# Kernel tuning notes

Measured on AMD Instinct MI355X. Metric: run time of the kernel, lower is better.

Reference implementation:

```python
import jax, jax.numpy as jnp
import numpy as np

BS, NE, F = 128, 512, 6
HEADS, DPH = 4, 4
N_EMBD = HEADS * DPH  # 16


def setup_inputs() -> dict:
    key = jax.random.key(0)
    k_inp, k_mask, kq, kk, kv, kp = jax.random.split(key, 6)
    inp = jax.random.normal(k_inp, (BS, NE, F), dtype=jnp.float32)
    # binary float mask; guarantee at least one unmasked entity per batch row
    mask = (jax.random.uniform(k_mask, (BS, NE)) < 0.8).astype(jnp.float32)
    mask = mask.at[:, 0].set(1.0)
    std = 1.0 / np.sqrt(N_EMBD)
    Wq = jax.random.normal(kq, (N_EMBD, F), dtype=jnp.float32) * std
    Wk = jax.random.normal(kk, (N_EMBD, F), dtype=jnp.float32) * std
    Wv = jax.random.normal(kv, (N_EMBD, F), dtype=jnp.float32) * std
    Wpost = jax.random.normal(kp, (F, N_EMBD), dtype=jnp.float32) * std
    return {"inp": inp, "mask": mask, "Wq": Wq, "Wk": Wk, "Wv": Wv, "Wpost": Wpost}


def reference(inp, mask, Wq, Wk, Wv, Wpost):
    bs, ne, f = inp.shape
    x_in = inp * mask[:, :, None]                       # mask input entities
    # projections (Linear with weight [out,in]): x @ W.T
    q = (x_in @ Wq.T).reshape(bs, ne, HEADS, DPH)
    k = (x_in @ Wk.T).reshape(bs, ne, HEADS, DPH)
    v = (x_in @ Wv.T).reshape(bs, ne, HEADS, DPH)
    scale = 1.0 / np.sqrt(N_EMBD / HEADS)               # 1/sqrt(4)
    logits = jnp.einsum('bqhd,bkhd->bhqk', q, k) * scale  # [bs,H,NE,NE]
    logits = logits + 1e9 * (mask[:, None, None, :] - 1.0)  # mask keys pre-softmax
    p = jax.nn.softmax(logits, axis=-1)
    p = p * mask[:, None, :, None]                      # zero masked query rows
    att = jnp.einsum('bhqk,bkhd->bqhd', p, v).reshape(bs, ne, N_EMBD)
    x = x_in + att @ Wpost.T                            # residual
    # mask-corrected mean/std normalization over dims [1,2]
    N = jnp.sum(mask, axis=1)[:, None, None]            # [bs,1,1] valid entity count
    mu = jnp.mean(x, axis=(1, 2), keepdims=True) * (ne / N)
    x2 = x + (1.0 - mask[:, :, None]) * mu              # fill masked slots with mu
    m2 = jnp.mean(x2, axis=(1, 2), keepdims=True)
    var = jnp.sum((x2 - m2) ** 2, axis=(1, 2), keepdims=True) / (ne * f - 1)  # unbiased
    std = jnp.sqrt(var) * jnp.sqrt((f * ne - 1.0) / (f * N - 1.0))
    xn = (x - mu) / (std + 1e-6)
    # masked mean pool over entities
    summed = jnp.sum(xn * mask[:, :, None], axis=1)     # [bs,F]
    denom = jnp.sum(mask, axis=1)[:, None]
    return summed / denom
```

## Files before the change

kernel.cpp:

```cpp
#include <hip/hip_runtime.h>
#include <math.h>

#define BS    128
#define NE    512
#define F     6
#define NH    4
#define DPH   4
#define NEMBD 16

#define CH    8
#define CPAD  65

#if __has_builtin(__builtin_amdgcn_exp2f)
#define EXP2(x) __builtin_amdgcn_exp2f(x)
#else
#define EXP2(x) exp2f(x)
#endif

typedef float v2f __attribute__((ext_vector_type(2)));

__global__ __launch_bounds__(512) void attn_kernel(
    const float* __restrict__ inp, const float* __restrict__ mask,
    const float* __restrict__ Wq, const float* __restrict__ Wk,
    const float* __restrict__ Wv, float* __restrict__ att_out)
{
    const int b    = blockIdx.x >> 2;
    const int h    = blockIdx.x & 3;
    const int t    = threadIdx.x;
    const int c    = t & 7;
    const int g    = t >> 3;
    const int w    = t >> 6;
    const int lane = t & 63;

    __shared__ float4 sk[CH * CPAD];
    __shared__ float4 sv[CH * CPAD];
    __shared__ float4 sq[576];
    __shared__ unsigned short rlist[512];
    __shared__ int wcnt[8];

    const float4 z4 = make_float4(0.f, 0.f, 0.f, 0.f);
    sk[c * CPAD + g] = z4;
    sv[c * CPAD + g] = z4;
    sq[9 * g + c]    = z4;

    const float me = mask[b * NE + t];
    const bool act = me > 0.f;

    const unsigned long long ball = __ballot(act);
    const int prefix = __builtin_amdgcn_mbcnt_hi((unsigned int)(ball >> 32),
                        __builtin_amdgcn_mbcnt_lo((unsigned int)ball, 0));
    if (lane == 0) wcnt[w] = (int)__popcll(ball);

    __syncthreads();

    int base = 0, Nk = 0;
    #pragma unroll
    for (int u = 0; u < 8; ++u) {
        const int cu = wcnt[u];
        Nk += cu;
        if (u < w) base += cu;
    }
    const int L = (Nk + 7) >> 3;
    const float lcorr = (float)(8 * L - Nk);

    if (act) {
        const int s = base + prefix;
        const float2* rp = (const float2*)(inp + ((size_t)(b * NE + t)) * F);
        const float2 r0 = rp[0], r1 = rp[1], r2 = rp[2];
        const float x0 = r0.x, x1 = r0.y, x2 = r1.x,
                    x3 = r1.y, x4 = r2.x, x5 = r2.y;
        const float* wk = Wk + h * DPH * F;
        const float* wv = Wv + h * DPH * F;
        const float* wq = Wq + h * DPH * F;
        const float QS = 0.5f * 1.44269504088896340736f;
        float kk[4], vv[4], qq[4];
        #pragma unroll
        for (int d = 0; d < DPH; ++d) {
            const float* wd = wk + d * F;
            kk[d] = x0*wd[0] + x1*wd[1] + x2*wd[2] + x3*wd[3] + x4*wd[4] + x5*wd[5];
            wd = wv + d * F;
            vv[d] = x0*wd[0] + x1*wd[1] + x2*wd[2] + x3*wd[3] + x4*wd[4] + x5*wd[5];
            wd = wq + d * F;
            qq[d] = QS * (x0*wd[0] + x1*wd[1] + x2*wd[2] + x3*wd[3] + x4*wd[4] + x5*wd[5]);
        }
        sk[(s & 7) * CPAD + (s >> 3)] = make_float4(kk[0], kk[1], kk[2], kk[3]);
        sv[(s & 7) * CPAD + (s >> 3)] = make_float4(vv[0], vv[1], vv[2], vv[3]);
        sq[9 * (s >> 3) + (s & 7)]    = make_float4(qq[0], qq[1], qq[2], qq[3]);
        rlist[s] = (unsigned short)t;
    }

    __syncthreads();

    if (64 * w >= Nk) return;

    float4 qa[8];
    #pragma unroll
    for (int r = 0; r < 8; ++r) qa[r] = sq[9 * g + r];
    v2f qv[4][DPH];
    #pragma unroll
    for (int p = 0; p < 4; ++p) {
        qv[p][0] = (v2f){qa[2*p].x, qa[2*p+1].x};
        qv[p][1] = (v2f){qa[2*p].y, qa[2*p+1].y};
        qv[p][2] = (v2f){qa[2*p].z, qa[2*p+1].z};
        qv[p][3] = (v2f){qa[2*p].w, qa[2*p+1].w};
    }

    const float4* kb = sk + c * CPAD;
    const float4* vb = sv + c * CPAD;
    v2f l2[4], a2[4][DPH];
    #pragma unroll
    for (int p = 0; p < 4; ++p) {
        l2[p] = (v2f)(0.f);
        #pragma unroll
        for (int d = 0; d < DPH; ++d) a2[p][d] = (v2f)(0.f);
    }

    #pragma unroll 4
    for (int j = 0; j < L; ++j) {
        const float4 kv = kb[j];
        const float4 uv = vb[j];
        const v2f kx = (v2f){kv.x, kv.x}, ky = (v2f){kv.y, kv.y},
                  kz = (v2f){kv.z, kv.z}, kw = (v2f){kv.w, kv.w};
        const v2f ux = (v2f){uv.x, uv.x}, uy = (v2f){uv.y, uv.y},
                  uz = (v2f){uv.z, uv.z}, uw = (v2f){uv.w, uv.w};
        #pragma unroll
        for (int p = 0; p < 4; ++p) {
            v2f s = qv[p][3] * kw;
            s = __builtin_elementwise_fma(qv[p][2], kz, s);
            s = __builtin_elementwise_fma(qv[p][1], ky, s);
            s = __builtin_elementwise_fma(qv[p][0], kx, s);
            v2f e;
            e.x = EXP2(s.x);
            e.y = EXP2(s.y);
            l2[p] += e;
            a2[p][0] = __builtin_elementwise_fma(e, ux, a2[p][0]);
            a2[p][1] = __builtin_elementwise_fma(e, uy, a2[p][1]);
            a2[p][2] = __builtin_elementwise_fma(e, uz, a2[p][2]);
            a2[p][3] = __builtin_elementwise_fma(e, uw, a2[p][3]);
        }
    }

    const int b0 = c & 1, b1 = (c >> 1) & 1, b2 = (c >> 2) & 1;

    float k1[5][4];
    #pragma unroll
    for (int p = 0; p < 4; ++p) {
        {
            const v2f v = l2[p];
            const float snd = b0 ? v.x : v.y;
            k1[0][p] = (b0 ? v.y : v.x) + __shfl_xor(snd, 1);
        }
        #pragma unroll
        for (int d = 0; d < DPH; ++d) {
            const v2f v = a2[p][d];
            const float snd = b0 ? v.x : v.y;
            k1[1 + d][p] = (b0 ? v.y : v.x) + __shfl_xor(snd, 1);
        }
    }

    float k2[5][2];
    #pragma unroll
    for (int v = 0; v < 5; ++v) {
        #pragma unroll
        for (int q = 0; q < 2; ++q) {
            const float keep = b1 ? k1[v][2*q + 1] : k1[v][2*q];
            const float snd  = b1 ? k1[v][2*q]     : k1[v][2*q + 1];
            k2[v][q] = keep + __shfl_xor(snd, 2);
        }
    }

    float fin[5];
    #pragma unroll
    for (int v = 0; v < 5; ++v) {
        const float keep = b2 ? k2[v][1] : k2[v][0];
        const float snd  = b2 ? k2[v][0] : k2[v][1];
        fin[v] = keep + __shfl_xor(snd, 4);
    }

    const int slot = 8 * g + c;
    if (slot < Nk) {
        const int row = rlist[slot];
        const float rs = 1.0f / (fin[0] - lcorr);
        float4* o = (float4*)(att_out + ((size_t)(b * NE + row)) * NEMBD + h * DPH);
        *o = make_float4(fin[1] * rs, fin[2] * rs, fin[3] * rs, fin[4] * rs);
    }
}

__global__ __launch_bounds__(NE) void epi_kernel(
    const float* __restrict__ inp, const float* __restrict__ mask,
    const float* __restrict__ Wpost, const float* __restrict__ att,
    float* __restrict__ out)
{
    const int b = blockIdx.x;
    const int i = threadIdx.x;
    const int wave = i >> 6;
    const int lane = i & 63;

    __shared__ float swp[F * NEMBD];
    __shared__ float red[64];

    if (i < F * NEMBD) swp[i] = Wpost[i];
    __syncthreads();

    const float mi = mask[b * NE + i];
    const float* row = inp + ((size_t)(b * NE + i)) * F;
    const float* ar  = att + ((size_t)(b * NE + i)) * NEMBD;

    float a[NEMBD];
    #pragma unroll
    for (int t = 0; t < NEMBD; t += 4) {
        const float4 v = *(const float4*)(ar + t);
        a[t] = v.x * mi; a[t+1] = v.y * mi; a[t+2] = v.z * mi; a[t+3] = v.w * mi;
    }

    float x[F];
    #pragma unroll
    for (int f = 0; f < F; ++f) {
        float acc = row[f] * mi;
        #pragma unroll
        for (int t = 0; t < NEMBD; ++t) acc = fmaf(a[t], swp[f * NEMBD + t], acc);
        x[f] = acc;
    }

    float rsum = x[0] + x[1] + x[2] + x[3] + x[4] + x[5];
    float rn = mi;
    #pragma unroll
    for (int off = 32; off >= 1; off >>= 1) {
        rsum += __shfl_down(rsum, off);
        rn   += __shfl_down(rn, off);
    }
    if (lane == 0) { red[wave * 2] = rsum; red[wave * 2 + 1] = rn; }
    __syncthreads();
    float S = 0.f, N = 0.f;
    #pragma unroll
    for (int w = 0; w < 8; ++w) { S += red[w * 2]; N += red[w * 2 + 1]; }

    const float mu     = S / (6.0f * N);
    const float sum_x2 = S + (NE - N) * 6.0f * mu;
    const float m2     = sum_x2 / (NE * 6.0f);
    const float add    = (1.0f - mi) * mu;

    float ss = 0.f;
    #pragma unroll
    for (int f = 0; f < F; ++f) { const float d = x[f] + add - m2; ss = fmaf(d, d, ss); }

    __syncthreads();
    #pragma unroll
    for (int off = 32; off >= 1; off >>= 1) ss += __shfl_down(ss, off);
    if (lane == 0) red[wave] = ss;
    __syncthreads();
    float vs = 0.f;
    #pragma unroll
    for (int w = 0; w < 8; ++w) vs += red[w];

    const float var  = vs / (NE * 6.0f - 1.0f);
    const float stdv = sqrtf(var) * sqrtf((6.0f * NE - 1.0f) / (6.0f * N - 1.0f));
    const float inv  = 1.0f / (stdv + 1e-6f);

    float y[F];
    #pragma unroll
    for (int f = 0; f < F; ++f) y[f] = mi * (x[f] - mu) * inv;

    __syncthreads();
    #pragma unroll
    for (int off = 32; off >= 1; off >>= 1) {
        #pragma unroll
        for (int f = 0; f < F; ++f) y[f] += __shfl_down(y[f], off);
    }
    if (lane == 0) {
        #pragma unroll
        for (int f = 0; f < F; ++f) red[wave * F + f] = y[f];
    }
    __syncthreads();
    if (i < F) {
        float tt = 0.f;
        #pragma unroll
        for (int w = 0; w < 8; ++w) tt += red[w * F + i];
        out[b * F + i] = tt / N;
    }
}

extern "C" void kernel_launch(void* const* d_in, const int* in_sizes, int n_in,
                              void* d_out, int out_size, void* d_ws, size_t ws_size,
                              hipStream_t stream) {
    const float* inp   = (const float*)d_in[0];
    const float* mask  = (const float*)d_in[1];
    const float* Wq    = (const float*)d_in[2];
    const float* Wk    = (const float*)d_in[3];
    const float* Wv    = (const float*)d_in[4];
    const float* Wpost = (const float*)d_in[5];
    float* out = (float*)d_out;
    float* att = (float*)d_ws;

    attn_kernel<<<BS * NH, 512, 0, stream>>>(inp, mask, Wq, Wk, Wv, att);
    epi_kernel <<<BS, NE, 0, stream>>>(inp, mask, Wpost, att, out);
}
```

Measured before the change: 94.86 us.

## Fuse attention and epilogue kernels via per-batch atomic last-block completion

Merges the attention kernel and the normalization/pooling epilogue into one launch. Each of the four head-blocks for a batch row increments a global atomic counter, and the last one to finish runs the epilogue on the attention output the others wrote to global memory. This removes one kernel launch and the gap between the two kernels. In exchange it adds threadfence/atomic overhead, serializes the epilogue onto a single block per batch row, and adds a min-blocks launch-bounds hint. Correctness depends on the counter being reset at the end of each call.

```diff
diff --git a/kernel.cpp b/kernel.cpp
--- a/kernel.cpp
+++ b/kernel.cpp
@@ -19,10 +19,13 @@
 
 typedef float v2f __attribute__((ext_vector_type(2)));
 
-__global__ __launch_bounds__(512) void attn_kernel(
+__device__ int g_ctr[BS];
+
+__global__ __launch_bounds__(512, 4) void fused_kernel(
     const float* __restrict__ inp, const float* __restrict__ mask,
     const float* __restrict__ Wq, const float* __restrict__ Wk,
-    const float* __restrict__ Wv, float* __restrict__ att_out)
+    const float* __restrict__ Wv, const float* __restrict__ Wpost,
+    float* __restrict__ att_out, float* __restrict__ out)
 {
     const int b    = blockIdx.x >> 2;
     const int h    = blockIdx.x & 3;
@@ -37,6 +40,9 @@
     __shared__ float4 sq[576];
     __shared__ unsigned short rlist[512];
     __shared__ int wcnt[8];
+    __shared__ float swp[F * NEMBD];
+    __shared__ float red[64];
+    __shared__ int s_old;
 
     const float4 z4 = make_float4(0.f, 0.f, 0.f, 0.f);
     sk[c * CPAD + g] = z4;
@@ -91,126 +97,121 @@
 
     __syncthreads();
 
-    if (64 * w >= Nk) return;
-
-    float4 qa[8];
-    #pragma unroll
-    for (int r = 0; r < 8; ++r) qa[r] = sq[9 * g + r];
-    v2f qv[4][DPH];
-    #pragma unroll
-    for (int p = 0; p < 4; ++p) {
-        qv[p][0] = (v2f){qa[2*p].x, qa[2*p+1].x};
-        qv[p][1] = (v2f){qa[2*p].y, qa[2*p+1].y};
-        qv[p][2] = (v2f){qa[2*p].z, qa[2*p+1].z};
-        qv[p][3] = (v2f){qa[2*p].w, qa[2*p+1].w};
-    }
-
-    const float4* kb = sk + c * CPAD;
-    const float4* vb = sv + c * CPAD;
-    v2f l2[4], a2[4][DPH];
-    #pragma unroll
-    for (int p = 0; p < 4; ++p) {
-        l2[p] = (v2f)(0.f);
-        #pragma unroll
-        for (int d = 0; d < DPH; ++d) a2[p][d] = (v2f)(0.f);
-    }
-
-    #pragma unroll 4
-    for (int j = 0; j < L; ++j) {
-        const float4 kv = kb[j];
-        const float4 uv = vb[j];
-        const v2f kx = (v2f){kv.x, kv.x}, ky = (v2f){kv.y, kv.y},
-                  kz = (v2f){kv.z, kv.z}, kw = (v2f){kv.w, kv.w};
-        const v2f ux = (v2f){uv.x, uv.x}, uy = (v2f){uv.y, uv.y},
-                  uz = (v2f){uv.z, uv.z}, uw = (v2f){uv.w, uv.w};
+    if (64 * w < Nk) {
+        float4 qa[8];
+        #pragma unroll
+        for (int r = 0; r < 8; ++r) qa[r] = sq[9 * g + r];
+        v2f qv[4][DPH];
         #pragma unroll
         for (int p = 0; p < 4; ++p) {
-            v2f s = qv[p][3] * kw;
-            s = __builtin_elementwise_fma(qv[p][2], kz, s);
-            s = __builtin_elementwise_fma(qv[p][1], ky, s);
-            s = __builtin_elementwise_fma(qv[p][0], kx, s);
-            v2f e;
-            e.x = EXP2(s.x);
-            e.y = EXP2(s.y);
-            l2[p] += e;
-            a2[p][0] = __builtin_elementwise_fma(e, ux, a2[p][0]);
-            a2[p][1] = __builtin_elementwise_fma(e, uy, a2[p][1]);
-            a2[p][2] = __builtin_elementwise_fma(e, uz, a2[p][2]);
-            a2[p][3] = __builtin_elementwise_fma(e, uw, a2[p][3]);
-        }
-    }
-
-    const int b0 = c & 1, b1 = (c >> 1) & 1, b2 = (c >> 2) & 1;
-
-    float k1[5][4];
-    #pragma unroll
-    for (int p = 0; p < 4; ++p) {
-        {
-            const v2f v = l2[p];
-            const float snd = b0 ? v.x : v.y;
-            k1[0][p] = (b0 ? v.y : v.x) + __shfl_xor(snd, 1);
-        }
-        #pragma unroll
-        for (int d = 0; d < DPH; ++d) {
-            const v2f v = a2[p][d];
-            const float snd = b0 ? v.x : v.y;
-            k1[1 + d][p] = (b0 ? v.y : v.x) + __shfl_xor(snd, 1);
-        }
-    }
-
-    float k2[5][2];
-    #pragma unroll
-    for (int v = 0; v < 5; ++v) {
-        #pragma unroll
-        for (int q = 0; q < 2; ++q) {
-            const float keep = b1 ? k1[v][2*q + 1] : k1[v][2*q];
-            const float snd  = b1 ? k1[v][2*q]     : k1[v][2*q + 1];
-            k2[v][q] = keep + __shfl_xor(snd, 2);
-        }
-    }
-
-    float fin[5];
-    #pragma unroll
-    for (int v = 0; v < 5; ++v) {
-        const float keep = b2 ? k2[v][1] : k2[v][0];
-        const float snd  = b2 ? k2[v][0] : k2[v][1];
-        fin[v] = keep + __shfl_xor(snd, 4);
-    }
-
-    const int slot = 8 * g + c;
-    if (slot < Nk) {
-        const int row = rlist[slot];
-        const float rs = 1.0f / (fin[0] - lcorr);
-        float4* o = (float4*)(att_out + ((size_t)(b * NE + row)) * NEMBD + h * DPH);
-        *o = make_float4(fin[1] * rs, fin[2] * rs, fin[3] * rs, fin[4] * rs);
-    }
-}
-
-__global__ __launch_bounds__(NE) void epi_kernel(
-    const float* __restrict__ inp, const float* __restrict__ mask,
-    const float* __restrict__ Wpost, const float* __restrict__ att,
-    float* __restrict__ out)
-{
-    const int b = blockIdx.x;
-    const int i = threadIdx.x;
-    const int wave = i >> 6;
-    const int lane = i & 63;
-
-    __shared__ float swp[F * NEMBD];
-    __shared__ float red[64];
-
-    if (i < F * NEMBD) swp[i] = Wpost[i];
-    __syncthreads();
-
-    const float mi = mask[b * NE + i];
-    const float* row = inp + ((size_t)(b * NE + i)) * F;
-    const float* ar  = att + ((size_t)(b * NE + i)) * NEMBD;
+            qv[p][0] = (v2f){qa[2*p].x, qa[2*p+1].x};
+            qv[p][1] = (v2f){qa[2*p].y, qa[2*p+1].y};
+            qv[p][2] = (v2f){qa[2*p].z, qa[2*p+1].z};
+            qv[p][3] = (v2f){qa[2*p].w, qa[2*p+1].w};
+        }
+
+        const float4* kb = sk + c * CPAD;
+        const float4* vb = sv + c * CPAD;
+        v2f l2[4], a2[4][DPH];
+        #pragma unroll
+        for (int p = 0; p < 4; ++p) {
+            l2[p] = (v2f)(0.f);
+            #pragma unroll
+            for (int d = 0; d < DPH; ++d) a2[p][d] = (v2f)(0.f);
+        }
+
+        #pragma unroll 4
+        for (int j = 0; j < L; ++j) {
+            const float4 kv = kb[j];
+            const float4 uv = vb[j];
+            const v2f kx = (v2f){kv.x, kv.x}, ky = (v2f){kv.y, kv.y},
+                      kz = (v2f){kv.z, kv.z}, kw = (v2f){kv.w, kv.w};
+            const v2f ux = (v2f){uv.x, uv.x}, uy = (v2f){uv.y, uv.y},
+                      uz = (v2f){uv.z, uv.z}, uw = (v2f){uv.w, uv.w};
+            #pragma unroll
+            for (int p = 0; p < 4; ++p) {
+                v2f s = qv[p][3] * kw;
+                s = __builtin_elementwise_fma(qv[p][2], kz, s);
+                s = __builtin_elementwise_fma(qv[p][1], ky, s);
+                s = __builtin_elementwise_fma(qv[p][0], kx, s);
+                v2f e;
+                e.x = EXP2(s.x);
+                e.y = EXP2(s.y);
+                l2[p] += e;
+                a2[p][0] = __builtin_elementwise_fma(e, ux, a2[p][0]);
+                a2[p][1] = __builtin_elementwise_fma(e, uy, a2[p][1]);
+                a2[p][2] = __builtin_elementwise_fma(e, uz, a2[p][2]);
+                a2[p][3] = __builtin_elementwise_fma(e, uw, a2[p][3]);
+            }
+        }
+
+        const int b0 = c & 1, b1 = (c >> 1) & 1, b2 = (c >> 2) & 1;
+
+        float k1[5][4];
+        #pragma unroll
+        for (int p = 0; p < 4; ++p) {
+            {
+                const v2f v = l2[p];
+                const float snd = b0 ? v.x : v.y;
+                k1[0][p] = (b0 ? v.y : v.x) + __shfl_xor(snd, 1);
+            }
+            #pragma unroll
+            for (int d = 0; d < DPH; ++d) {
+                const v2f v = a2[p][d];
+                const float snd = b0 ? v.x : v.y;
+                k1[1 + d][p] = (b0 ? v.y : v.x) + __shfl_xor(snd, 1);
+            }
+        }
+
+        float k2[5][2];
+        #pragma unroll
+        for (int v = 0; v < 5; ++v) {
+            #pragma unroll
+            for (int q = 0; q < 2; ++q) {
+                const float keep = b1 ? k1[v][2*q + 1] : k1[v][2*q];
+                const float snd  = b1 ? k1[v][2*q]     : k1[v][2*q + 1];
+                k2[v][q] = keep + __shfl_xor(snd, 2);
+            }
+        }
+
+        float fin[5];
+        #pragma unroll
+        for (int v = 0; v < 5; ++v) {
+            const float keep = b2 ? k2[v][1] : k2[v][0];
+            const float snd  = b2 ? k2[v][0] : k2[v][1];
+            fin[v] = keep + __shfl_xor(snd, 4);
+        }
+
+        const int slot = 8 * g + c;
+        if (slot < Nk) {
+            const int row = rlist[slot];
+            const float rs = 1.0f / (fin[0] - lcorr);
+            float4* o = (float4*)(att_out + ((size_t)(b * NE + row)) * NEMBD + h * DPH);
+            *o = make_float4(fin[1] * rs, fin[2] * rs, fin[3] * rs, fin[4] * rs);
+        }
+    }
+
+    __syncthreads();
+    if (t == 0) {
+        __threadfence();
+        s_old = atomicAdd(&g_ctr[b], 1);
+    }
+    __syncthreads();
+    if (s_old != NH - 1) return;
+    __threadfence();
+
+    if (t < F * NEMBD) swp[t] = Wpost[t];
+    __syncthreads();
+
+    const float mi = me;
+    const float* row = inp + ((size_t)(b * NE + t)) * F;
+    const float* ar  = att_out + ((size_t)(b * NE + t)) * NEMBD;
 
     float a[NEMBD];
     #pragma unroll
-    for (int t = 0; t < NEMBD; t += 4) {
-        const float4 v = *(const float4*)(ar + t);
-        a[t] = v.x * mi; a[t+1] = v.y * mi; a[t+2] = v.z * mi; a[t+3] = v.w * mi;
+    for (int u = 0; u < NEMBD; u += 4) {
+        const float4 v = *(const float4*)(ar + u);
+        a[u] = v.x * mi; a[u+1] = v.y * mi; a[u+2] = v.z * mi; a[u+3] = v.w * mi;
     }
 
     float x[F];
@@ -218,7 +219,7 @@
     for (int f = 0; f < F; ++f) {
         float acc = row[f] * mi;
         #pragma unroll
-        for (int t = 0; t < NEMBD; ++t) acc = fmaf(a[t], swp[f * NEMBD + t], acc);
+        for (int u = 0; u < NEMBD; ++u) acc = fmaf(a[u], swp[f * NEMBD + u], acc);
         x[f] = acc;
     }
 
@@ -229,11 +230,11 @@
         rsum += __shfl_down(rsum, off);
         rn   += __shfl_down(rn, off);
     }
-    if (lane == 0) { red[wave * 2] = rsum; red[wave * 2 + 1] = rn; }
+    if (lane == 0) { red[w * 2] = rsum; red[w * 2 + 1] = rn; }
     __syncthreads();
     float S = 0.f, N = 0.f;
     #pragma unroll
-    for (int w = 0; w < 8; ++w) { S += red[w * 2]; N += red[w * 2 + 1]; }
+    for (int u = 0; u < 8; ++u) { S += red[u * 2]; N += red[u * 2 + 1]; }
 
     const float mu     = S / (6.0f * N);
     const float sum_x2 = S + (NE - N) * 6.0f * mu;
@@ -247,11 +248,11 @@
     __syncthreads();
     #pragma unroll
     for (int off = 32; off >= 1; off >>= 1) ss += __shfl_down(ss, off);
-    if (lane == 0) red[wave] = ss;
+    if (lane == 0) red[w] = ss;
     __syncthreads();
     float vs = 0.f;
     #pragma unroll
-    for (int w = 0; w < 8; ++w) vs += red[w];
+    for (int u = 0; u < 8; ++u) vs += red[u];
 
     const float var  = vs / (NE * 6.0f - 1.0f);
     const float stdv = sqrtf(var) * sqrtf((6.0f * NE - 1.0f) / (6.0f * N - 1.0f));
@@ -269,15 +270,17 @@
     }
     if (lane == 0) {
         #pragma unroll
-        for (int f = 0; f < F; ++f) red[wave * F + f] = y[f];
-    }
-    __syncthreads();
-    if (i < F) {
+        for (int f = 0; f < F; ++f) red[w * F + f] = y[f];
+    }
+    __syncthreads();
+    if (t < F) {
         float tt = 0.f;
         #pragma unroll
-        for (int w = 0; w < 8; ++w) tt += red[w * F + i];
-        out[b * F + i] = tt / N;
-    }
+        for (int u = 0; u < 8; ++u) tt += red[u * F + t];
+        out[b * F + t] = tt / N;
+    }
+
+    if (t == 0) atomicExch(&g_ctr[b], 0);
 }
 
 extern "C" void kernel_launch(void* const* d_in, const int* in_sizes, int n_in,
@@ -292,6 +295,5 @@
     float* out = (float*)d_out;
     float* att = (float*)d_ws;
 
-    attn_kernel<<<BS * NH, 512, 0, stream>>>(inp, mask, Wq, Wk, Wv, att);
-    epi_kernel <<<BS, NE, 0, stream>>>(inp, mask, Wpost, att, out);
+    fused_kernel<<<BS * NH, 512, 0, stream>>>(inp, mask, Wq, Wk, Wv, Wpost, att, out);
 }
```

Measured after the change: 144.9 us. 52.8% more time.
